# Kernel tuning notes

Hardware: AMD Instinct MI355X
Metric: run time of the kernel (lower is better)

Reference implementation:

```python
import jax, jax.numpy as jnp
import numpy as np

N = 50000
E = 600000
P = 100000
IN_FEATS = 128
HIDDEN = 128


def _glorot(key, shape):
    fan_in, fan_out = shape[0], shape[1]
    lim = np.sqrt(6.0 / (fan_in + fan_out)).astype(np.float32)
    return jax.random.uniform(key, shape, jnp.float32, -lim, lim)


def setup_inputs() -> dict:
    key = jax.random.key(0)
    ks = jax.random.split(key, 20)
    inp = {
        "x": jax.random.normal(ks[0], (N, IN_FEATS), jnp.float32),
        "edge_src": jax.random.randint(ks[1], (E,), 0, N, jnp.int32),
        "edge_dst": jax.random.randint(ks[2], (E,), 0, N, jnp.int32),
        "pos_src": jax.random.randint(ks[3], (P,), 0, N, jnp.int32),
        "pos_dst": jax.random.randint(ks[4], (P,), 0, N, jnp.int32),
        "neg_src": jax.random.randint(ks[5], (P,), 0, N, jnp.int32),
        "neg_dst": jax.random.randint(ks[6], (P,), 0, N, jnp.int32),
        # SAGEConv layer 1 (in_feats -> hidden)
        "Ws1": _glorot(ks[7], (IN_FEATS, HIDDEN)),
        "Wn1": _glorot(ks[8], (IN_FEATS, HIDDEN)),
        "b1": jnp.zeros((HIDDEN,), jnp.float32),
        # SAGEConv layer 2 (hidden -> hidden)
        "Ws2": _glorot(ks[9], (HIDDEN, HIDDEN)),
        "Wn2": _glorot(ks[10], (HIDDEN, HIDDEN)),
        "b2": jnp.zeros((HIDDEN,), jnp.float32),
        # EdgeDecoder MLP: Linear-ReLU-Linear-ReLU-Linear(->1)
        "Wd1": _glorot(ks[11], (HIDDEN, HIDDEN)),
        "bd1": jnp.zeros((HIDDEN,), jnp.float32),
        "Wd2": _glorot(ks[12], (HIDDEN, HIDDEN)),
        "bd2": jnp.zeros((HIDDEN,), jnp.float32),
        "Wd3": _glorot(ks[13], (HIDDEN, 1)),
        "bd3": jnp.zeros((1,), jnp.float32),
    }
    return inp


def _sage_conv(h, src, dst, Ws, Wn, b):
    # mean aggregation over incoming neighbors, then fc_self + fc_neigh + bias
    msg = h[src]                                             # [E, d]
    agg = jax.ops.segment_sum(msg, dst, num_segments=N)      # [N, d]
    deg = jax.ops.segment_sum(jnp.ones((src.shape[0],), h.dtype), dst,
                              num_segments=N)
    mean = agg / jnp.maximum(deg, 1.0)[:, None]
    return h @ Ws + mean @ Wn + b


def _decode(h, src, dst, Wd1, bd1, Wd2, bd2, Wd3, bd3):
    z = h[src] * h[dst]                                      # [P, d]
    z = jax.nn.relu(z @ Wd1 + bd1)
    z = jax.nn.relu(z @ Wd2 + bd2)
    return z @ Wd3 + bd3                                     # [P, 1]


def reference(x, edge_src, edge_dst, pos_src, pos_dst, neg_src, neg_dst,
              Ws1, Wn1, b1, Ws2, Wn2, b2, Wd1, bd1, Wd2, bd2, Wd3, bd3):
    h = jax.nn.relu(_sage_conv(x, edge_src, edge_dst, Ws1, Wn1, b1))
    h = _sage_conv(h, edge_src, edge_dst, Ws2, Wn2, b2)  # last layer: no act
    h_pos = _decode(h, pos_src, pos_dst, Wd1, bd1, Wd2, bd2, Wd3, bd3)
    h_neg = _decode(h, neg_src, neg_dst, Wd1, bd1, Wd2, bd2, Wd3, bd3)
    return (h_pos, h_neg)
```

## Files before the change

### kernel.cpp

```cpp
#include <hip/hip_runtime.h>
#include <hip/hip_bf16.h>

#define N_NODES 50000
#define N_EDGES 600000
#define N_PAIRS 100000

typedef __attribute__((ext_vector_type(8))) short bf16x8;
typedef __attribute__((ext_vector_type(4))) float f32x4;

__device__ inline unsigned short f2b(float f) {
    unsigned u = __float_as_uint(f);
    unsigned r = u + 0x7fff + ((u >> 16) & 1);
    return (unsigned short)(r >> 16);
}
__device__ inline float b2f(unsigned short h) {
    return __uint_as_float(((unsigned)h) << 16);
}

__global__ void k_prep(const float* __restrict__ x, unsigned short* __restrict__ A1,
                       unsigned short* __restrict__ xb16,
                       const int* __restrict__ edge_dst, int* __restrict__ deg,
                       const float* __restrict__ Ws1, const float* __restrict__ Wn1,
                       const float* __restrict__ Ws2, const float* __restrict__ Wn2,
                       const float* __restrict__ Wd1, const float* __restrict__ Wd2,
                       unsigned short* __restrict__ WT1, unsigned short* __restrict__ WT2,
                       unsigned short* __restrict__ WdT1, unsigned short* __restrict__ WdT2) {
    int idx = blockIdx.x * blockDim.x + threadIdx.x;
    if (idx < N_EDGES) atomicAdd(&deg[edge_dst[idx]], 1);
    if (idx < 98304) {
        int id = idx;
        if (id < 32768) {
            int j = id & 7, g = id >> 3;
            int lane = g & 63, t = g >> 6;
            int ct = t & 7, kb = t >> 3;
            int k = kb * 32 + (lane >> 4) * 8 + j, n = ct * 16 + (lane & 15);
            float v = (k < 128) ? Ws1[k * 128 + n] : Wn1[(k - 128) * 128 + n];
            WT1[id] = f2b(v);
        } else if (id < 65536) {
            int r = id - 32768;
            int j = r & 7, g = r >> 3;
            int lane = g & 63, t = g >> 6;
            int ct = t & 7, kb = t >> 3;
            int k = kb * 32 + (lane >> 4) * 8 + j, n = ct * 16 + (lane & 15);
            float v = (k < 128) ? Ws2[k * 128 + n] : Wn2[(k - 128) * 128 + n];
            WT2[r] = f2b(v);
        } else if (id < 81920) {
            int r = id - 65536;
            int j = r & 7, g = r >> 3;
            int lane = g & 63, t = g >> 6;
            int ct = t & 7, kb = t >> 3;
            int k = kb * 32 + (lane >> 4) * 8 + j, n = ct * 16 + (lane & 15);
            WdT1[r] = f2b(Wd1[k * 128 + n]);
        } else {
            int r = id - 81920;
            int j = r & 7, g = r >> 3;
            int lane = g & 63, t = g >> 6;
            int ct = t & 7, kb = t >> 3;
            int k = kb * 32 + (lane >> 4) * 8 + j, n = ct * 16 + (lane & 15);
            WdT2[r] = f2b(Wd2[k * 128 + n]);
        }
    }
    if (idx >= N_NODES * 32) return;
    int row = idx >> 5, c4 = (idx & 31) * 4;
    float4 v = *(const float4*)(x + row * 128 + c4);
    unsigned lo = (unsigned)f2b(v.x) | ((unsigned)f2b(v.y) << 16);
    unsigned hi = (unsigned)f2b(v.z) | ((unsigned)f2b(v.w) << 16);
    uint2 o; o.x = lo; o.y = hi;
    *(uint2*)(A1 + row * 256 + c4) = o;
    *(uint2*)(xb16 + row * 128 + c4) = o;
}

__global__ void k_scan1(const int* __restrict__ deg, int* __restrict__ row_ptr,
                        int* __restrict__ bsum, int n) {
    __shared__ int tmp[1024];
    int i = blockIdx.x * 1024 + threadIdx.x;
    int d = (i < n) ? deg[i] : 0;
    tmp[threadIdx.x] = d;
    __syncthreads();
    int run = d;
    for (int off = 1; off < 1024; off <<= 1) {
        int t = (threadIdx.x >= off) ? tmp[threadIdx.x - off] : 0;
        __syncthreads();
        run += t;
        tmp[threadIdx.x] = run;
        __syncthreads();
    }
    if (i < n) row_ptr[i] = run - d;
    if (threadIdx.x == 1023) bsum[blockIdx.x] = run;
}

__global__ void k_add(int* __restrict__ row_ptr, int* __restrict__ cursor,
                      const int* __restrict__ bsum, int n) {
    __shared__ int prefix;
    if (threadIdx.x == 0) {
        int acc = 0;
        for (int j = 0; j < (int)blockIdx.x; j++) acc += bsum[j];
        prefix = acc;
    }
    __syncthreads();
    int i = blockIdx.x * 1024 + threadIdx.x;
    if (i < n) {
        int v = row_ptr[i] + prefix;
        row_ptr[i] = v;
        cursor[i] = v;
    }
    if (i == 0) row_ptr[n] = N_EDGES;
}

__global__ void k_scatter(const int* __restrict__ src, const int* __restrict__ dst,
                          int* __restrict__ cursor, int* __restrict__ colA) {
    int e = blockIdx.x * blockDim.x + threadIdx.x;
    if (e < N_EDGES) {
        int d = dst[e];
        int slot = atomicAdd(&cursor[d], 1);
        colA[slot] = src[e];
    }
}

__global__ __launch_bounds__(256) void k_agg(const unsigned short* __restrict__ hb, int ldh,
                                             const int* __restrict__ row_ptr,
                                             const int* __restrict__ colA,
                                             unsigned short* __restrict__ outm, int ldo) {
    int wave = (blockIdx.x * blockDim.x + threadIdx.x) >> 6;
    int lane = threadIdx.x & 63;
    int q = lane >> 4, ql = lane & 15;
    int w = wave * 4 + q;
    if (w >= N_NODES) w = N_NODES - 1;
    int s = row_ptr[w], e = row_ptr[w + 1];
    float a[8];
#pragma unroll
    for (int j = 0; j < 8; j++) a[j] = 0.f;
    for (int base = s; base < e; base += 16) {
        int ce = (base + ql < e) ? colA[base + ql] : 0;
        int cnt = min(16, e - base);
        int ei[16];
#pragma unroll
        for (int j = 0; j < 16; j++) {
            int sl = (j < cnt) ? j : (cnt - 1);
            ei[j] = __shfl(ce, (q << 4) + sl, 64);
        }
        uint4 v[16];
#pragma unroll
        for (int j = 0; j < 16; j++)
            v[j] = *(const uint4*)(hb + (size_t)ei[j] * ldh + ql * 8);
#pragma unroll
        for (int j = 0; j < 16; j += 2) {
            const unsigned* p0 = (const unsigned*)&v[j];
            const unsigned* p1 = (const unsigned*)&v[j + 1];
            if (j + 1 < cnt) {
#pragma unroll
                for (int t = 0; t < 4; t++) {
                    a[2 * t] += b2f(p0[t] & 0xffff) + b2f(p1[t] & 0xffff);
                    a[2 * t + 1] += b2f(p0[t] >> 16) + b2f(p1[t] >> 16);
                }
            } else if (j < cnt) {
#pragma unroll
                for (int t = 0; t < 4; t++) {
                    a[2 * t] += b2f(p0[t] & 0xffff);
                    a[2 * t + 1] += b2f(p0[t] >> 16);
                }
            }
        }
    }
    float rd = 1.0f / (float)max(e - s, 1);
    uint4 o;
    unsigned* op = (unsigned*)&o;
#pragma unroll
    for (int t = 0; t < 4; t++)
        op[t] = (unsigned)f2b(a[2 * t] * rd) | ((unsigned)f2b(a[2 * t + 1] * rd) << 16);
    *(uint4*)(outm + (size_t)w * ldo + ql * 8) = o;
}

__global__ __launch_bounds__(256) void k_gemm(const unsigned short* __restrict__ A, int lda, int K,
                                              const unsigned short* __restrict__ BT,
                                              const float* __restrict__ bias,
                                              unsigned short* __restrict__ Hout, int ldo,
                                              int M, int relu) {
    __shared__ unsigned short ot[128][136];
    int wv = threadIdx.x >> 6, lane = threadIdx.x & 63;
    int lr = lane & 15, lq = lane >> 4;
    int r0 = blockIdx.x * 128 + wv * 32;
    int arow0 = min(r0 + lr, M - 1);
    int arow1 = min(r0 + 16 + lr, M - 1);
    f32x4 acc[2][8];
    f32x4 zero = {0.f, 0.f, 0.f, 0.f};
#pragma unroll
    for (int m = 0; m < 2; m++)
#pragma unroll
        for (int ct = 0; ct < 8; ct++) acc[m][ct] = zero;
    for (int kb = 0; kb < K; kb += 32) {
        int ka = kb + lq * 8;
        int kbi = kb >> 5;
        bf16x8 wf[8];
#pragma unroll
        for (int ct = 0; ct < 8; ct++)
            wf[ct] = *(const bf16x8*)(BT + ((size_t)(kbi * 8 + ct) * 64 + lane) * 8);
        bf16x8 af0 = *(const bf16x8*)(A + (size_t)arow0 * lda + ka);
        bf16x8 af1 = *(const bf16x8*)(A + (size_t)arow1 * lda + ka);
#pragma unroll
        for (int ct = 0; ct < 8; ct++) {
            acc[0][ct] = __builtin_amdgcn_mfma_f32_16x16x32_bf16(af0, wf[ct], acc[0][ct], 0, 0, 0);
            acc[1][ct] = __builtin_amdgcn_mfma_f32_16x16x32_bf16(af1, wf[ct], acc[1][ct], 0, 0, 0);
        }
    }
#pragma unroll
    for (int m = 0; m < 2; m++) {
#pragma unroll
        for (int ct = 0; ct < 8; ct++) {
            int colc = ct * 16 + lr;
            float bv = bias[colc];
#pragma unroll
            for (int r = 0; r < 4; r++) {
                float v = acc[m][ct][r] + bv;
                if (relu) v = fmaxf(v, 0.f);
                ot[wv * 32 + m * 16 + lq * 4 + r][colc] = f2b(v);
            }
        }
    }
    __syncthreads();
    int tid = threadIdx.x;
    int rr = tid >> 2, cc = tid & 3;
#pragma unroll
    for (int half = 0; half < 2; half++) {
        int row = half * 64 + rr;
        int grow = blockIdx.x * 128 + row;
        if (grow < M) {
#pragma unroll
            for (int c = 0; c < 4; c++) {
                int so = c * 32 + cc * 8;
                *(uint4*)(Hout + (size_t)grow * ldo + so) = *(const uint4*)(&ot[row][so]);
            }
        }
    }
}

__global__ __launch_bounds__(512, 2) void k_mlp(const unsigned short* __restrict__ h2b,
                                                const int* __restrict__ pos_src,
                                                const int* __restrict__ pos_dst,
                                                const int* __restrict__ neg_src,
                                                const int* __restrict__ neg_dst,
                                                const unsigned short* __restrict__ WdT1,
                                                const unsigned short* __restrict__ WdT2,
                                                const float* __restrict__ bd1,
                                                const float* __restrict__ bd2,
                                                const float* __restrict__ Wd3,
                                                const float* __restrict__ bd3,
                                                float* __restrict__ out, int P2) {
    __shared__ unsigned short wds[32768];
    __shared__ unsigned short t1[8][32][136];
    const int tid = threadIdx.x;
    {
        const uint4* s1 = (const uint4*)WdT1;
        const uint4* s2 = (const uint4*)WdT2;
        uint4* d = (uint4*)wds;
#pragma unroll
        for (int i = 0; i < 4; i++) d[tid + i * 512] = s1[tid + i * 512];
#pragma unroll
        for (int i = 0; i < 4; i++) d[2048 + tid + i * 512] = s2[tid + i * 512];
    }
    __syncthreads();
    const unsigned short* wd1 = wds;
    const unsigned short* wd2 = wds + 16384;
    const int wv = tid >> 6;
    const int lane = tid & 63, lr = lane & 15, lq = lane >> 4;
    const int nw = gridDim.x << 3;
    const int nt = P2 >> 5;

    uint4 z[16];
    auto ISSUE = [&](int tile) {
        const int row0 = tile * 32;
        int p0 = min(row0 + lr, P2 - 1);
        int p1 = min(row0 + 16 + lr, P2 - 1);
        int s0i = (p0 < N_PAIRS) ? pos_src[p0] : neg_src[p0 - N_PAIRS];
        int d0i = (p0 < N_PAIRS) ? pos_dst[p0] : neg_dst[p0 - N_PAIRS];
        int s1i = (p1 < N_PAIRS) ? pos_src[p1] : neg_src[p1 - N_PAIRS];
        int d1i = (p1 < N_PAIRS) ? pos_dst[p1] : neg_dst[p1 - N_PAIRS];
#pragma unroll
        for (int kb = 0; kb < 4; kb++) {
            int ka = kb * 32 + lq * 8;
            z[kb]      = *(const uint4*)(h2b + (size_t)s0i * 128 + ka);
            z[4 + kb]  = *(const uint4*)(h2b + (size_t)d0i * 128 + ka);
            z[8 + kb]  = *(const uint4*)(h2b + (size_t)s1i * 128 + ka);
            z[12 + kb] = *(const uint4*)(h2b + (size_t)d1i * 128 + ka);
        }
    };

    bf16x8 af0[4], af1[4];
    auto REPACK = [&]() {
#pragma unroll
        for (int kb = 0; kb < 4; kb++) {
            unsigned r0v[4], r1v[4];
            const unsigned* a0p = (const unsigned*)&z[kb];
            const unsigned* b0p = (const unsigned*)&z[4 + kb];
            const unsigned* a1p = (const unsigned*)&z[8 + kb];
            const unsigned* b1p = (const unsigned*)&z[12 + kb];
#pragma unroll
            for (int j = 0; j < 4; j++) {
                unsigned short lo0 = f2b(b2f(a0p[j] & 0xffff) * b2f(b0p[j] & 0xffff));
                unsigned short hi0 = f2b(b2f(a0p[j] >> 16) * b2f(b0p[j] >> 16));
                r0v[j] = (unsigned)lo0 | ((unsigned)hi0 << 16);
                unsigned short lo1 = f2b(b2f(a1p[j] & 0xffff) * b2f(b1p[j] & 0xffff));
                unsigned short hi1 = f2b(b2f(a1p[j] >> 16) * b2f(b1p[j] >> 16));
                r1v[j] = (unsigned)lo1 | ((unsigned)hi1 << 16);
            }
            af0[kb] = *(const bf16x8*)r0v;
            af1[kb] = *(const bf16x8*)r1v;
        }
    };

    auto COMPUTE_REST = [&](int tile) {
        const int row0 = tile * 32;
        f32x4 zero = {0.f, 0.f, 0.f, 0.f};
        f32x4 acc[2][8];
#pragma unroll
        for (int m = 0; m < 2; m++)
#pragma unroll
            for (int ct = 0; ct < 8; ct++) acc[m][ct] = zero;
#pragma unroll
        for (int kb = 0; kb < 4; kb++) {
            bf16x8 wf[8];
#pragma unroll
            for (int ct = 0; ct < 8; ct++)
                wf[ct] = *(const bf16x8*)(wd1 + ((kb * 8 + ct) * 64 + lane) * 8);
#pragma unroll
            for (int ct = 0; ct < 8; ct++) {
                acc[0][ct] = __builtin_amdgcn_mfma_f32_16x16x32_bf16(af0[kb], wf[ct], acc[0][ct], 0, 0, 0);
                acc[1][ct] = __builtin_amdgcn_mfma_f32_16x16x32_bf16(af1[kb], wf[ct], acc[1][ct], 0, 0, 0);
            }
        }
#pragma unroll
        for (int m = 0; m < 2; m++)
#pragma unroll
            for (int ct = 0; ct < 8; ct++) {
                int colc = ct * 16 + lr;
                float bv = bd1[colc];
#pragma unroll
                for (int r = 0; r < 4; r++) {
                    float v = fmaxf(acc[m][ct][r] + bv, 0.f);
                    t1[wv][m * 16 + lq * 4 + r][colc] = f2b(v);
                }
            }
        asm volatile("s_waitcnt lgkmcnt(0)" ::: "memory");
#pragma unroll
        for (int m = 0; m < 2; m++)
#pragma unroll
            for (int ct = 0; ct < 8; ct++) acc[m][ct] = zero;
#pragma unroll
        for (int kb = 0; kb < 4; kb++) {
            int ka = kb * 32 + lq * 8;
            bf16x8 wf[8];
#pragma unroll
            for (int ct = 0; ct < 8; ct++)
                wf[ct] = *(const bf16x8*)(wd2 + ((kb * 8 + ct) * 64 + lane) * 8);
            bf16x8 bf0 = *(const bf16x8*)(&t1[wv][lr][ka]);
            bf16x8 bf1 = *(const bf16x8*)(&t1[wv][16 + lr][ka]);
#pragma unroll
            for (int ct = 0; ct < 8; ct++) {
                acc[0][ct] = __builtin_amdgcn_mfma_f32_16x16x32_bf16(bf0, wf[ct], acc[0][ct], 0, 0, 0);
                acc[1][ct] = __builtin_amdgcn_mfma_f32_16x16x32_bf16(bf1, wf[ct], acc[1][ct], 0, 0, 0);
            }
        }
        float sc[2][4] = {{0.f, 0.f, 0.f, 0.f}, {0.f, 0.f, 0.f, 0.f}};
#pragma unroll
        for (int ct = 0; ct < 8; ct++) {
            int colc = ct * 16 + lr;
            float bv = bd2[colc];
            float w3 = Wd3[colc];
#pragma unroll
            for (int m = 0; m < 2; m++)
#pragma unroll
                for (int r = 0; r < 4; r++) {
                    float v = fmaxf(acc[m][ct][r] + bv, 0.f);
                    sc[m][r] += v * w3;
                }
        }
#pragma unroll
        for (int mm = 1; mm < 16; mm <<= 1)
#pragma unroll
            for (int m = 0; m < 2; m++)
#pragma unroll
                for (int r = 0; r < 4; r++) sc[m][r] += __shfl_xor(sc[m][r], mm, 64);
        if (lr == 0) {
            float b3 = bd3[0];
#pragma unroll
            for (int m = 0; m < 2; m++)
#pragma unroll
                for (int r = 0; r < 4; r++) {
                    int g = row0 + m * 16 + lq * 4 + r;
                    if (g < P2) out[g] = sc[m][r] + b3;
                }
        }
    };

    int t = blockIdx.x * 8 + wv;
    if (t >= nt) return;
    ISSUE(t);
    while (true) {
        REPACK();
        int tn = t + nw;
        if (tn < nt) ISSUE(tn);
        COMPUTE_REST(t);
        if (tn >= nt) break;
        t = tn;
    }
}

static inline size_t alignup(size_t v) { return (v + 255) & ~(size_t)255; }

extern "C" void kernel_launch(void* const* d_in, const int* in_sizes, int n_in,
                              void* d_out, int out_size, void* d_ws, size_t ws_size,
                              hipStream_t stream) {
    const float* x = (const float*)d_in[0];
    const int* edge_src = (const int*)d_in[1];
    const int* edge_dst = (const int*)d_in[2];
    const int* pos_src = (const int*)d_in[3];
    const int* pos_dst = (const int*)d_in[4];
    const int* neg_src = (const int*)d_in[5];
    const int* neg_dst = (const int*)d_in[6];
    const float* Ws1 = (const float*)d_in[7];
    const float* Wn1 = (const float*)d_in[8];
    const float* b1 = (const float*)d_in[9];
    const float* Ws2 = (const float*)d_in[10];
    const float* Wn2 = (const float*)d_in[11];
    const float* b2 = (const float*)d_in[12];
    const float* Wd1 = (const float*)d_in[13];
    const float* bd1 = (const float*)d_in[14];
    const float* Wd2 = (const float*)d_in[15];
    const float* bd2 = (const float*)d_in[16];
    const float* Wd3 = (const float*)d_in[17];
    const float* bd3 = (const float*)d_in[18];
    float* out = (float*)d_out;

    char* p = (char*)d_ws;
    int* deg = (int*)p;            p += alignup(N_NODES * 4);
    int* row_ptr = (int*)p;        p += alignup((N_NODES + 1) * 4);
    int* cursor = (int*)p;         p += alignup(N_NODES * 4);
    int* bsum = (int*)p;           p += alignup(64 * 4);
    int* colA = (int*)p;           p += alignup(N_EDGES * 4);
    unsigned short* A1 = (unsigned short*)p;  p += alignup((size_t)N_NODES * 256 * 2);
    unsigned short* A2 = (unsigned short*)p;  p += alignup((size_t)N_NODES * 256 * 2);
    unsigned short* h2b = (unsigned short*)p; p += alignup((size_t)N_NODES * 128 * 2);
    unsigned short* WT1 = (unsigned short*)p;  p += alignup(32768 * 2);
    unsigned short* WT2 = (unsigned short*)p;  p += alignup(32768 * 2);
    unsigned short* WdT1 = (unsigned short*)p; p += alignup(16384 * 2);
    unsigned short* WdT2 = (unsigned short*)p; p += alignup(16384 * 2);
    unsigned short* xb16 = h2b;

    hipMemsetAsync(deg, 0, N_NODES * 4, stream);

    k_prep<<<(N_NODES * 32 + 255) / 256, 256, 0, stream>>>(
        x, A1, xb16, edge_dst, deg,
        Ws1, Wn1, Ws2, Wn2, Wd1, Wd2, WT1, WT2, WdT1, WdT2);

    int nb1 = (N_NODES + 1023) / 1024;
    k_scan1<<<nb1, 1024, 0, stream>>>(deg, row_ptr, bsum, N_NODES);
    k_add<<<nb1, 1024, 0, stream>>>(row_ptr, cursor, bsum, N_NODES);
    k_scatter<<<(N_EDGES + 255) / 256, 256, 0, stream>>>(edge_src, edge_dst, cursor, colA);

    int nagg = (N_NODES + 15) / 16;

    k_agg<<<nagg, 256, 0, stream>>>(xb16, 128, row_ptr, colA, A1 + 128, 256);
    k_gemm<<<(N_NODES + 127) / 128, 256, 0, stream>>>(A1, 256, 256, WT1, b1, A2, 256, N_NODES, 1);

    k_agg<<<nagg, 256, 0, stream>>>(A2, 256, row_ptr, colA, A2 + 128, 256);
    k_gemm<<<(N_NODES + 127) / 128, 256, 0, stream>>>(A2, 256, 256, WT2, b2, h2b, 128, N_NODES, 0);

    k_mlp<<<256, 512, 0, stream>>>(h2b, pos_src, pos_dst, neg_src, neg_dst,
                                   WdT1, WdT2, bd1, bd2, Wd3, bd3,
                                   out, N_PAIRS * 2);
}
```

Measured before the change: 278.5 us.

## Fuse neighbor mean aggregation with SAGE GEMM via shared-memory tile

```diff
diff --git a/kernel.cpp b/kernel.cpp
--- a/kernel.cpp
+++ b/kernel.cpp
@@ -17,8 +17,7 @@
     return __uint_as_float(((unsigned)h) << 16);
 }
 
-__global__ void k_prep(const float* __restrict__ x, unsigned short* __restrict__ A1,
-                       unsigned short* __restrict__ xb16,
+__global__ void k_prep(const float* __restrict__ x, unsigned short* __restrict__ xb16,
                        const int* __restrict__ edge_dst, int* __restrict__ deg,
                        const float* __restrict__ Ws1, const float* __restrict__ Wn1,
                        const float* __restrict__ Ws2, const float* __restrict__ Wn2,
@@ -66,7 +65,6 @@
     unsigned lo = (unsigned)f2b(v.x) | ((unsigned)f2b(v.y) << 16);
     unsigned hi = (unsigned)f2b(v.z) | ((unsigned)f2b(v.w) << 16);
     uint2 o; o.x = lo; o.y = hi;
-    *(uint2*)(A1 + row * 256 + c4) = o;
     *(uint2*)(xb16 + row * 128 + c4) = o;
 }
 
@@ -117,119 +115,114 @@
     }
 }
 
-__global__ __launch_bounds__(256) void k_agg(const unsigned short* __restrict__ hb, int ldh,
-                                             const int* __restrict__ row_ptr,
-                                             const int* __restrict__ colA,
-                                             unsigned short* __restrict__ outm, int ldo) {
-    int wave = (blockIdx.x * blockDim.x + threadIdx.x) >> 6;
-    int lane = threadIdx.x & 63;
-    int q = lane >> 4, ql = lane & 15;
-    int w = wave * 4 + q;
-    if (w >= N_NODES) w = N_NODES - 1;
-    int s = row_ptr[w], e = row_ptr[w + 1];
-    float a[8];
-#pragma unroll
-    for (int j = 0; j < 8; j++) a[j] = 0.f;
-    for (int base = s; base < e; base += 16) {
-        int ce = (base + ql < e) ? colA[base + ql] : 0;
-        int cnt = min(16, e - base);
-        int ei[16];
-#pragma unroll
-        for (int j = 0; j < 16; j++) {
-            int sl = (j < cnt) ? j : (cnt - 1);
-            ei[j] = __shfl(ce, (q << 4) + sl, 64);
-        }
-        uint4 v[16];
-#pragma unroll
-        for (int j = 0; j < 16; j++)
-            v[j] = *(const uint4*)(hb + (size_t)ei[j] * ldh + ql * 8);
-#pragma unroll
-        for (int j = 0; j < 16; j += 2) {
-            const unsigned* p0 = (const unsigned*)&v[j];
-            const unsigned* p1 = (const unsigned*)&v[j + 1];
-            if (j + 1 < cnt) {
-#pragma unroll
-                for (int t = 0; t < 4; t++) {
-                    a[2 * t] += b2f(p0[t] & 0xffff) + b2f(p1[t] & 0xffff);
-                    a[2 * t + 1] += b2f(p0[t] >> 16) + b2f(p1[t] >> 16);
+__global__ __launch_bounds__(512) void k_fused(const unsigned short* __restrict__ selfB,
+                                               const int* __restrict__ row_ptr,
+                                               const int* __restrict__ colA,
+                                               const unsigned short* __restrict__ BT,
+                                               const float* __restrict__ bias,
+                                               unsigned short* __restrict__ Hout,
+                                               int M, int relu) {
+    __shared__ unsigned short mt[128][136];
+    const int tid = threadIdx.x;
+    const int wv = tid >> 6, lane = tid & 63;
+    const int q = lane >> 4, ql = lane & 15;
+    const int r0 = blockIdx.x * 128;
+
+#pragma unroll 1
+    for (int round = 0; round < 4; round++) {
+        int i = round * 32 + wv * 4 + q;
+        int w = r0 + i;
+        bool act = (w < M);
+        int wc = min(w, M - 1);
+        int s = row_ptr[wc], e = row_ptr[wc + 1];
+        float a[8];
+#pragma unroll
+        for (int j = 0; j < 8; j++) a[j] = 0.f;
+        for (int base = s; base < e; base += 16) {
+            int ce = (base + ql < e) ? colA[base + ql] : 0;
+            int cnt = min(16, e - base);
+            int ei[16];
+#pragma unroll
+            for (int j = 0; j < 16; j++) {
+                int sl = (j < cnt) ? j : (cnt - 1);
+                ei[j] = __shfl(ce, (q << 4) + sl, 64);
+            }
+            uint4 v[16];
+#pragma unroll
+            for (int j = 0; j < 16; j++)
+                v[j] = *(const uint4*)(selfB + (size_t)ei[j] * 128 + ql * 8);
+#pragma unroll
+            for (int j = 0; j < 16; j += 2) {
+                const unsigned* p0 = (const unsigned*)&v[j];
+                const unsigned* p1 = (const unsigned*)&v[j + 1];
+                if (j + 1 < cnt) {
+#pragma unroll
+                    for (int t = 0; t < 4; t++) {
+                        a[2 * t] += b2f(p0[t] & 0xffff) + b2f(p1[t] & 0xffff);
+                        a[2 * t + 1] += b2f(p0[t] >> 16) + b2f(p1[t] >> 16);
+                    }
+                } else if (j < cnt) {
+#pragma unroll
+                    for (int t = 0; t < 4; t++) {
+                        a[2 * t] += b2f(p0[t] & 0xffff);
+                        a[2 * t + 1] += b2f(p0[t] >> 16);
+                    }
                 }
-            } else if (j < cnt) {
-#pragma unroll
-                for (int t = 0; t < 4; t++) {
-                    a[2 * t] += b2f(p0[t] & 0xffff);
-                    a[2 * t + 1] += b2f(p0[t] >> 16);
-                }
-            }
-        }
-    }
-    float rd = 1.0f / (float)max(e - s, 1);
-    uint4 o;
-    unsigned* op = (unsigned*)&o;
-#pragma unroll
-    for (int t = 0; t < 4; t++)
-        op[t] = (unsigned)f2b(a[2 * t] * rd) | ((unsigned)f2b(a[2 * t + 1] * rd) << 16);
-    *(uint4*)(outm + (size_t)w * ldo + ql * 8) = o;
-}
-
-__global__ __launch_bounds__(256) void k_gemm(const unsigned short* __restrict__ A, int lda, int K,
-                                              const unsigned short* __restrict__ BT,
-                                              const float* __restrict__ bias,
-                                              unsigned short* __restrict__ Hout, int ldo,
-                                              int M, int relu) {
-    __shared__ unsigned short ot[128][136];
-    int wv = threadIdx.x >> 6, lane = threadIdx.x & 63;
-    int lr = lane & 15, lq = lane >> 4;
-    int r0 = blockIdx.x * 128 + wv * 32;
-    int arow0 = min(r0 + lr, M - 1);
-    int arow1 = min(r0 + 16 + lr, M - 1);
-    f32x4 acc[2][8];
+            }
+        }
+        float rd = 1.0f / (float)max(e - s, 1);
+        uint4 o;
+        unsigned* op = (unsigned*)&o;
+#pragma unroll
+        for (int t = 0; t < 4; t++)
+            op[t] = (unsigned)f2b(a[2 * t] * rd) | ((unsigned)f2b(a[2 * t + 1] * rd) << 16);
+        if (act) *(uint4*)(&mt[i][ql * 8]) = o;
+    }
+    __syncthreads();
+
+    const int lr = lane & 15, lq = lane >> 4;
+    const int rw0 = r0 + wv * 16;
+    const int arow = min(rw0 + lr, M - 1);
+    f32x4 acc[8];
     f32x4 zero = {0.f, 0.f, 0.f, 0.f};
 #pragma unroll
-    for (int m = 0; m < 2; m++)
-#pragma unroll
-        for (int ct = 0; ct < 8; ct++) acc[m][ct] = zero;
-    for (int kb = 0; kb < K; kb += 32) {
-        int ka = kb + lq * 8;
-        int kbi = kb >> 5;
+    for (int ct = 0; ct < 8; ct++) acc[ct] = zero;
+#pragma unroll
+    for (int kbi = 0; kbi < 8; kbi++) {
         bf16x8 wf[8];
 #pragma unroll
         for (int ct = 0; ct < 8; ct++)
             wf[ct] = *(const bf16x8*)(BT + ((size_t)(kbi * 8 + ct) * 64 + lane) * 8);
-        bf16x8 af0 = *(const bf16x8*)(A + (size_t)arow0 * lda + ka);
-        bf16x8 af1 = *(const bf16x8*)(A + (size_t)arow1 * lda + ka);
-#pragma unroll
-        for (int ct = 0; ct < 8; ct++) {
-            acc[0][ct] = __builtin_amdgcn_mfma_f32_16x16x32_bf16(af0, wf[ct], acc[0][ct], 0, 0, 0);
-            acc[1][ct] = __builtin_amdgcn_mfma_f32_16x16x32_bf16(af1, wf[ct], acc[1][ct], 0, 0, 0);
-        }
-    }
-#pragma unroll
-    for (int m = 0; m < 2; m++) {
-#pragma unroll
-        for (int ct = 0; ct < 8; ct++) {
-            int colc = ct * 16 + lr;
-            float bv = bias[colc];
-#pragma unroll
-            for (int r = 0; r < 4; r++) {
-                float v = acc[m][ct][r] + bv;
-                if (relu) v = fmaxf(v, 0.f);
-                ot[wv * 32 + m * 16 + lq * 4 + r][colc] = f2b(v);
-            }
-        }
-    }
-    __syncthreads();
-    int tid = threadIdx.x;
+        bf16x8 af;
+        if (kbi < 4) {
+            af = *(const bf16x8*)(selfB + (size_t)arow * 128 + kbi * 32 + lq * 8);
+        } else {
+            af = *(const bf16x8*)(&mt[arow - r0][(kbi - 4) * 32 + lq * 8]);
+        }
+#pragma unroll
+        for (int ct = 0; ct < 8; ct++)
+            acc[ct] = __builtin_amdgcn_mfma_f32_16x16x32_bf16(af, wf[ct], acc[ct], 0, 0, 0);
+    }
+    __syncthreads();
+#pragma unroll
+    for (int ct = 0; ct < 8; ct++) {
+        int colc = ct * 16 + lr;
+        float bv = bias[colc];
+#pragma unroll
+        for (int r = 0; r < 4; r++) {
+            float v = acc[ct][r] + bv;
+            if (relu) v = fmaxf(v, 0.f);
+            mt[wv * 16 + lq * 4 + r][colc] = f2b(v);
+        }
+    }
+    __syncthreads();
     int rr = tid >> 2, cc = tid & 3;
-#pragma unroll
-    for (int half = 0; half < 2; half++) {
-        int row = half * 64 + rr;
-        int grow = blockIdx.x * 128 + row;
-        if (grow < M) {
-#pragma unroll
-            for (int c = 0; c < 4; c++) {
-                int so = c * 32 + cc * 8;
-                *(uint4*)(Hout + (size_t)grow * ldo + so) = *(const uint4*)(&ot[row][so]);
-            }
+    int grow = r0 + rr;
+    if (grow < M) {
+#pragma unroll
+        for (int c = 0; c < 4; c++) {
+            int so = c * 32 + cc * 8;
+            *(uint4*)(Hout + (size_t)grow * 128 + so) = *(const uint4*)(&mt[rr][so]);
         }
     }
 }
@@ -437,8 +430,7 @@
     int* cursor = (int*)p;         p += alignup(N_NODES * 4);
     int* bsum = (int*)p;           p += alignup(64 * 4);
     int* colA = (int*)p;           p += alignup(N_EDGES * 4);
-    unsigned short* A1 = (unsigned short*)p;  p += alignup((size_t)N_NODES * 256 * 2);
-    unsigned short* A2 = (unsigned short*)p;  p += alignup((size_t)N_NODES * 256 * 2);
+    unsigned short* h1 = (unsigned short*)p;  p += alignup((size_t)N_NODES * 128 * 2);
     unsigned short* h2b = (unsigned short*)p; p += alignup((size_t)N_NODES * 128 * 2);
     unsigned short* WT1 = (unsigned short*)p;  p += alignup(32768 * 2);
     unsigned short* WT2 = (unsigned short*)p;  p += alignup(32768 * 2);
@@ -449,7 +441,7 @@
     hipMemsetAsync(deg, 0, N_NODES * 4, stream);
 
     k_prep<<<(N_NODES * 32 + 255) / 256, 256, 0, stream>>>(
-        x, A1, xb16, edge_dst, deg,
+        x, xb16, edge_dst, deg,
         Ws1, Wn1, Ws2, Wn2, Wd1, Wd2, WT1, WT2, WdT1, WdT2);
 
     int nb1 = (N_NODES + 1023) / 1024;
@@ -457,13 +449,10 @@
     k_add<<<nb1, 1024, 0, stream>>>(row_ptr, cursor, bsum, N_NODES);
     k_scatter<<<(N_EDGES + 255) / 256, 256, 0, stream>>>(edge_src, edge_dst, cursor, colA);
 
-    int nagg = (N_NODES + 15) / 16;
-
-    k_agg<<<nagg, 256, 0, stream>>>(xb16, 128, row_ptr, colA, A1 + 128, 256);
-    k_gemm<<<(N_NODES + 127) / 128, 256, 0, stream>>>(A1, 256, 256, WT1, b1, A2, 256, N_NODES, 1);
-
-    k_agg<<<nagg, 256, 0, stream>>>(A2, 256, row_ptr, colA, A2 + 128, 256);
-    k_gemm<<<(N_NODES + 127) / 128, 256, 0, stream>>>(A2, 256, 256, WT2, b2, h2b, 128, N_NODES, 0);
+    int nblk = (N_NODES + 127) / 128;
+
+    k_fused<<<nblk, 512, 0, stream>>>(xb16, row_ptr, colA, WT1, b1, h1, N_NODES, 1);
+    k_fused<<<nblk, 512, 0, stream>>>(h1, row_ptr, colA, WT2, b2, h2b, N_NODES, 0);
 
     k_mlp<<<256, 512, 0, stream>>>(h2b, pos_src, pos_dst, neg_src, neg_dst,
                                    WdT1, WdT2, bd1, bd2, Wd3, bd3,
```

Result: no change. 274.7 us (-1.3%).
